# Performance work log

Hardware: AMD Instinct MI355X
Metric: run time of the kernel (lower is better)

## Reference

```python
import jax, jax.numpy as jnp
import numpy as np

N_NODES = 100000
NEG_SLOPE = 0.2  # PyG GATConv default


def gat_conv(x, src, dst, W, a_src, a_dst, n_nodes):
    """One PyG-style GATConv (with self-loops already appended to src/dst).
    x: [N, Fin], W: [Fin, H*C], a_src/a_dst: [H, C]. Returns [N, H, C]."""
    H, C = a_src.shape
    h = (x @ W).reshape(-1, H, C)                      # [N, H, C]
    s_src = jnp.einsum('nhc,hc->nh', h, a_src)         # [N, H]
    s_dst = jnp.einsum('nhc,hc->nh', h, a_dst)         # [N, H]
    e = jax.nn.leaky_relu(s_src[src] + s_dst[dst], NEG_SLOPE)  # [E, H]
    # segment softmax over incoming edges of each destination node
    e_max = jax.ops.segment_max(e, dst, num_segments=n_nodes)  # [N, H]
    e_exp = jnp.exp(e - e_max[dst])
    denom = jax.ops.segment_sum(e_exp, dst, num_segments=n_nodes)
    alpha = e_exp / (denom[dst] + 1e-16)               # [E, H]
    msg = h[src] * alpha[:, :, None]                   # [E, H, C]
    return jax.ops.segment_sum(msg, dst, num_segments=n_nodes)  # [N, H, C]


def setup_inputs() -> dict:
    key = jax.random.key(0)
    ks = jax.random.split(key, 10)
    in_dim, hidden, heads, out_dim = 128, 32, 4, 32
    N, E = N_NODES, 1600000
    x = jax.random.normal(ks[0], (N, in_dim), dtype=jnp.float32)
    edge_index = jax.random.randint(ks[1], (2, E), 0, N, dtype=jnp.int64)
    s = 0.1
    return {
        'x': x,
        'edge_index': edge_index,
        'W1': s * jax.random.normal(ks[2], (in_dim, heads * hidden), dtype=jnp.float32),
        'a_src1': s * jax.random.normal(ks[3], (heads, hidden), dtype=jnp.float32),
        'a_dst1': s * jax.random.normal(ks[4], (heads, hidden), dtype=jnp.float32),
        'b1': jnp.zeros((heads * hidden,), dtype=jnp.float32),
        'W2': s * jax.random.normal(ks[5], (heads * hidden, out_dim), dtype=jnp.float32),
        'a_src2': s * jax.random.normal(ks[6], (1, out_dim), dtype=jnp.float32),
        'a_dst2': s * jax.random.normal(ks[7], (1, out_dim), dtype=jnp.float32),
        'b2': jnp.zeros((out_dim,), dtype=jnp.float32),
    }


def reference(x, edge_index, W1, a_src1, a_dst1, b1, W2, a_src2, a_dst2, b2):
    N = x.shape[0]
    loops = jnp.arange(N, dtype=edge_index.dtype)
    src = jnp.concatenate([edge_index[0], loops])  # PyG adds self-loops
    dst = jnp.concatenate([edge_index[1], loops])
    h1 = gat_conv(x, src, dst, W1, a_src1, a_dst1, N)      # [N, H, C]
    h1 = jax.nn.elu(h1.reshape(N, -1) + b1)                # concat heads + bias, elu
    h2 = gat_conv(h1, src, dst, W2, a_src2, a_dst2, N)     # [N, 1, out]
    return h2.mean(axis=1) + b2                            # concat=False -> mean over heads
```

## Files before the change

kernel.cpp:

```cpp
#include <hip/hip_runtime.h>
#include <hip/hip_bf16.h>

#define NEG 0.2f
#define BK_SHIFT 9
#define BK_CAP 9216

typedef short short8 __attribute__((ext_vector_type(8)));
typedef float f32x4 __attribute__((ext_vector_type(4)));

__device__ __forceinline__ float lrelu(float x){ return x > 0.f ? x : NEG * x; }
__device__ __forceinline__ float elu_f(float x){ return x > 0.f ? x : expm1f(x); }
__device__ __forceinline__ unsigned short f2bf(float f){
  unsigned int u = __float_as_uint(f);
  unsigned int r = u + 0x7fffu + ((u >> 16) & 1u);
  return (unsigned short)(r >> 16);
}
__device__ __forceinline__ float bf2f(unsigned short u){
  return __uint_as_float(((unsigned int)u) << 16);
}

__global__ __launch_bounds__(256) void k_binA(
    const int* __restrict__ src, const int* __restrict__ dst, int E,
    int* __restrict__ gcursor, int2* __restrict__ ebuf){
  __shared__ int hist[256];
  __shared__ int base[256];
  int t = threadIdx.x;
  hist[t] = 0;
  __syncthreads();
  int e0 = blockIdx.x * 4096;
  for (int j = 0; j < 16; j++){
    int e = e0 + j * 256 + t;
    if (e < E) atomicAdd(&hist[dst[e] >> BK_SHIFT], 1);
  }
  __syncthreads();
  int cnt = hist[t];
  if (cnt > 0) base[t] = atomicAdd(&gcursor[t], cnt);
  hist[t] = 0;
  __syncthreads();
  for (int j = 0; j < 16; j++){
    int e = e0 + j * 256 + t;
    if (e < E){
      int d = dst[e]; int b = d >> BK_SHIFT;
      int loc = atomicAdd(&hist[b], 1);
      ebuf[(size_t)b * BK_CAP + base[b] + loc] = make_int2(src[e], d);
    }
  }
}

__global__ __launch_bounds__(256) void k_bscan(
    const int* __restrict__ gcount, int* __restrict__ bbase,
    int* __restrict__ rowp, int N, int NBK, int total){
  __shared__ int sd[256];
  int t = threadIdx.x;
  int nodes = 0;
  if (t < NBK){ int nb = N - (t << BK_SHIFT); nodes = nb > 512 ? 512 : nb; }
  int v = (t < NBK) ? gcount[t] + nodes : 0;
  sd[t] = v; __syncthreads();
  for (int off = 1; off < 256; off <<= 1){
    int x = (t >= off) ? sd[t - off] : 0;
    __syncthreads(); sd[t] += x; __syncthreads();
  }
  if (t < NBK) bbase[t] = sd[t] - v;
  if (t == 0) rowp[N] = total;
}

__global__ __launch_bounds__(256) void k_csrB2(
    const int2* __restrict__ ebuf, const int* __restrict__ gcount,
    const int* __restrict__ bbase, int* __restrict__ rowp,
    int* __restrict__ csr, int N){
  __shared__ int hist[512];
  __shared__ int psum[256];
  int b = blockIdx.x, t = threadIdx.x;
  int nbase = b << BK_SHIFT;
  int cnt = gcount[b];
  const int2* eb = ebuf + (size_t)b * BK_CAP;
  hist[t] = 0; hist[t + 256] = 0;
  __syncthreads();
  for (int i = t; i < cnt; i += 256)
    atomicAdd(&hist[eb[i].y - nbase], 1);
  __syncthreads();
  int v0 = hist[2 * t], v1 = hist[2 * t + 1];
  int ps = v0 + v1;
  psum[t] = ps; __syncthreads();
  for (int off = 1; off < 256; off <<= 1){
    int x = (t >= off) ? psum[t - off] : 0;
    __syncthreads(); psum[t] += x; __syncthreads();
  }
  int eo = psum[t] - ps;
  int bb = bbase[b];
  int n0 = 2 * t, n1 = 2 * t + 1;
  int r0 = bb + eo + n0;
  int r1 = bb + eo + v0 + n1;
  if (nbase + n0 < N) rowp[nbase + n0] = r0;
  if (nbase + n1 < N) rowp[nbase + n1] = r1;
  __syncthreads();
  hist[n0] = r0; hist[n1] = r1;
  __syncthreads();
  for (int i = t; i < cnt; i += 256){
    int2 e = eb[i];
    int pos = atomicAdd(&hist[e.y - nbase], 1);
    csr[pos] = e.x;
  }
  __syncthreads();
  if (nbase + n0 < N) csr[hist[n0]] = nbase + n0;
  if (nbase + n1 < N) csr[hist[n1]] = nbase + n1;
}

__global__ __launch_bounds__(256, 3) void k_gemm1(
    const float* __restrict__ x, const float* __restrict__ W,
    const float* __restrict__ a_src, const float* __restrict__ a_dst,
    unsigned short* __restrict__ h_bf, float* __restrict__ ss, float* __restrict__ sd, int N){
  __shared__ unsigned short Wt[128 * 136];
  __shared__ unsigned short Xb[64 * 136];
  int t = threadIdx.x;
  int rb = blockIdx.x * 64;

  {
    int n = t & 127, kh = (t >> 7) << 6;
    #pragma unroll
    for (int j = 0; j < 16; j++){
      int k0 = kh + j * 4;
      float w0 = W[(size_t)(k0 + 0) * 128 + n];
      float w1 = W[(size_t)(k0 + 1) * 128 + n];
      float w2 = W[(size_t)(k0 + 2) * 128 + n];
      float w3 = W[(size_t)(k0 + 3) * 128 + n];
      uint2 pk;
      pk.x = ((unsigned)f2bf(w1) << 16) | f2bf(w0);
      pk.y = ((unsigned)f2bf(w3) << 16) | f2bf(w2);
      *(uint2*)&Wt[n * 136 + k0] = pk;
    }
  }
  #pragma unroll
  for (int j = 0; j < 8; j++){
    int fi = j * 256 + t;
    int row = fi >> 5, k4 = (fi & 31) * 4;
    int gr = rb + row;
    float4 v = make_float4(0.f, 0.f, 0.f, 0.f);
    if (gr < N) v = *(const float4*)&x[(size_t)gr * 128 + k4];
    uint2 pk;
    pk.x = ((unsigned)f2bf(v.y) << 16) | f2bf(v.x);
    pk.y = ((unsigned)f2bf(v.w) << 16) | f2bf(v.z);
    *(uint2*)&Xb[row * 136 + k4] = pk;
  }
  __syncthreads();

  int w = t >> 6, l = t & 63;
  int m = l & 15, quad = l >> 4;
  f32x4 acc[8];
  #pragma unroll
  for (int ct = 0; ct < 8; ct++) acc[ct] = (f32x4){0.f, 0.f, 0.f, 0.f};

  #pragma unroll
  for (int kc = 0; kc < 4; kc++){
    short8 a = *(const short8*)&Xb[(w * 16 + m) * 136 + kc * 32 + quad * 8];
    #pragma unroll
    for (int ct = 0; ct < 8; ct++){
      short8 b = *(const short8*)&Wt[(ct * 16 + m) * 136 + kc * 32 + quad * 8];
      acc[ct] = __builtin_amdgcn_mfma_f32_16x16x32_bf16(a, b, acc[ct], 0, 0, 0);
    }
  }

  float as[8], ad[8];
  #pragma unroll
  for (int ct = 0; ct < 8; ct++){ as[ct] = a_src[ct * 16 + m]; ad[ct] = a_dst[ct * 16 + m]; }

  #pragma unroll
  for (int reg = 0; reg < 4; reg++){
    int gr = rb + w * 16 + quad * 4 + reg;
    bool ok = gr < N;
    if (ok){
      #pragma unroll
      for (int ct = 0; ct < 8; ct++)
        h_bf[(size_t)gr * 128 + ct * 16 + m] = f2bf(acc[ct][reg]);
    }
    #pragma unroll
    for (int hh = 0; hh < 4; hh++){
      float ps = acc[2*hh][reg] * as[2*hh] + acc[2*hh+1][reg] * as[2*hh+1];
      float pd = acc[2*hh][reg] * ad[2*hh] + acc[2*hh+1][reg] * ad[2*hh+1];
      ps += __shfl_xor(ps, 1, 16); ps += __shfl_xor(ps, 2, 16);
      ps += __shfl_xor(ps, 4, 16); ps += __shfl_xor(ps, 8, 16);
      pd += __shfl_xor(pd, 1, 16); pd += __shfl_xor(pd, 2, 16);
      pd += __shfl_xor(pd, 4, 16); pd += __shfl_xor(pd, 8, 16);
      if (m == 0 && ok){ ss[(size_t)gr * 4 + hh] = ps; sd[(size_t)gr * 4 + hh] = pd; }
    }
  }
}

__global__ __launch_bounds__(256) void k_agg1(
    const int* __restrict__ row_ptr, const int* __restrict__ csr_src,
    const float* __restrict__ ss, const float* __restrict__ sdst,
    const __hip_bfloat162* __restrict__ hb2,
    unsigned int* __restrict__ out1_bf, int N){
  int n = blockIdx.x * 4 + (threadIdx.x >> 6);
  if (n >= N) return;
  int l = threadIdx.x & 63;
  int hd = l >> 4;
  float sdv = sdst[(size_t)n * 4 + hd];
  int j8 = l & 7, hh8 = (l >> 3) & 3;
  float sw8 = sdst[(size_t)n * 4 + hh8];
  int j4 = l & 3, hh4 = (l >> 2) & 3;
  float sw4 = sdst[(size_t)n * 4 + hh4];
  int beg = row_ptr[n], end = row_ptr[n + 1];
  float ax = 0.f, ay = 0.f, sw = 0.f;
  int e = beg;
  for (; e + 8 <= end; e += 8){
    int sj = csr_src[e + j8];
    float wv = __expf(lrelu(ss[(size_t)sj * 4 + hh8] + sw8));
    int s0 = __shfl(sj, 0, 8), s1 = __shfl(sj, 1, 8), s2 = __shfl(sj, 2, 8), s3 = __shfl(sj, 3, 8);
    int s4 = __shfl(sj, 4, 8), s5 = __shfl(sj, 5, 8), s6 = __shfl(sj, 6, 8), s7 = __shfl(sj, 7, 8);
    float w0 = __shfl(wv, hd * 8 + 0, 32), w1 = __shfl(wv, hd * 8 + 1, 32);
    float w2 = __shfl(wv, hd * 8 + 2, 32), w3 = __shfl(wv, hd * 8 + 3, 32);
    float w4 = __shfl(wv, hd * 8 + 4, 32), w5 = __shfl(wv, hd * 8 + 5, 32);
    float w6 = __shfl(wv, hd * 8 + 6, 32), w7 = __shfl(wv, hd * 8 + 7, 32);
    float2 v0 = __bfloat1622float2(hb2[(size_t)s0 * 64 + l]);
    float2 v1 = __bfloat1622float2(hb2[(size_t)s1 * 64 + l]);
    float2 v2 = __bfloat1622float2(hb2[(size_t)s2 * 64 + l]);
    float2 v3 = __bfloat1622float2(hb2[(size_t)s3 * 64 + l]);
    float2 v4 = __bfloat1622float2(hb2[(size_t)s4 * 64 + l]);
    float2 v5 = __bfloat1622float2(hb2[(size_t)s5 * 64 + l]);
    float2 v6 = __bfloat1622float2(hb2[(size_t)s6 * 64 + l]);
    float2 v7 = __bfloat1622float2(hb2[(size_t)s7 * 64 + l]);
    ax += w0*v0.x + w1*v1.x + w2*v2.x + w3*v3.x + w4*v4.x + w5*v5.x + w6*v6.x + w7*v7.x;
    ay += w0*v0.y + w1*v1.y + w2*v2.y + w3*v3.y + w4*v4.y + w5*v5.y + w6*v6.y + w7*v7.y;
    sw += w0 + w1 + w2 + w3 + w4 + w5 + w6 + w7;
  }
  for (; e + 4 <= end; e += 4){
    int sj = csr_src[e + j4];
    float wv = __expf(lrelu(ss[(size_t)sj * 4 + hh4] + sw4));
    int s0 = __shfl(sj, 0, 4), s1 = __shfl(sj, 1, 4);
    int s2 = __shfl(sj, 2, 4), s3 = __shfl(sj, 3, 4);
    float w0 = __shfl(wv, hd * 4 + 0, 16), w1 = __shfl(wv, hd * 4 + 1, 16);
    float w2 = __shfl(wv, hd * 4 + 2, 16), w3 = __shfl(wv, hd * 4 + 3, 16);
    float2 v0 = __bfloat1622float2(hb2[(size_t)s0 * 64 + l]);
    float2 v1 = __bfloat1622float2(hb2[(size_t)s1 * 64 + l]);
    float2 v2 = __bfloat1622float2(hb2[(size_t)s2 * 64 + l]);
    float2 v3 = __bfloat1622float2(hb2[(size_t)s3 * 64 + l]);
    ax += w0*v0.x + w1*v1.x + w2*v2.x + w3*v3.x;
    ay += w0*v0.y + w1*v1.y + w2*v2.y + w3*v3.y;
    sw += w0 + w1 + w2 + w3;
  }
  for (; e < end; e++){
    int s = csr_src[e];
    float w = __expf(lrelu(ss[(size_t)s * 4 + hd] + sdv));
    float2 v = __bfloat1622float2(hb2[(size_t)s * 64 + l]);
    ax += w*v.x; ay += w*v.y; sw += w;
  }
  float inv = 1.f / (sw + 1e-16f);
  unsigned int lo = f2bf(ax * inv), hi = f2bf(ay * inv);
  out1_bf[(size_t)n * 64 + l] = (hi << 16) | lo;
}

__global__ __launch_bounds__(256) void k_gemm2(
    const unsigned int* __restrict__ out1_bf, const float* __restrict__ b1,
    const float* __restrict__ W2,
    const float* __restrict__ a_src, const float* __restrict__ a_dst,
    unsigned short* __restrict__ h2_bf, float* __restrict__ s_src2, float* __restrict__ s_dst2, int N){
  __shared__ __align__(16) float Wl[128 * 32];
  __shared__ __align__(16) float Xl[64 * 132];
  int t = threadIdx.x;
  int rb = blockIdx.x * 64;

  const float4* Wg4 = (const float4*)W2;
  float4* Wl4 = (float4*)Wl;
  #pragma unroll
  for (int j = 0; j < 4; j++) Wl4[j * 256 + t] = Wg4[j * 256 + t];

  #pragma unroll
  for (int j = 0; j < 4; j++){
    int fi = j * 256 + t;
    int row = fi >> 4, q = fi & 15;
    int gr = rb + row;
    float v[8] = {0.f,0.f,0.f,0.f,0.f,0.f,0.f,0.f};
    if (gr < N){
      uint4 u = *(const uint4*)&out1_bf[(size_t)gr * 64 + q * 4];
      float4 bva = *(const float4*)&b1[q * 8];
      float4 bvb = *(const float4*)&b1[q * 8 + 4];
      v[0] = elu_f(bf2f((unsigned short)(u.x & 0xffff)) + bva.x);
      v[1] = elu_f(bf2f((unsigned short)(u.x >> 16))    + bva.y);
      v[2] = elu_f(bf2f((unsigned short)(u.y & 0xffff)) + bva.z);
      v[3] = elu_f(bf2f((unsigned short)(u.y >> 16))    + bva.w);
      v[4] = elu_f(bf2f((unsigned short)(u.z & 0xffff)) + bvb.x);
      v[5] = elu_f(bf2f((unsigned short)(u.z >> 16))    + bvb.y);
      v[6] = elu_f(bf2f((unsigned short)(u.w & 0xffff)) + bvb.z);
      v[7] = elu_f(bf2f((unsigned short)(u.w >> 16))    + bvb.w);
    }
    #pragma unroll
    for (int i = 0; i < 8; i++) Xl[row * 132 + q * 8 + i] = v[i];
  }
  __syncthreads();

  int cg = t & 7, rg = t >> 3;
  int c0 = cg * 4, r0 = rg * 2;
  float acc[2][4] = {};

  #pragma unroll 8
  for (int k = 0; k < 128; k++){
    float a0 = Xl[r0 * 132 + k];
    float a1 = Xl[(r0 + 1) * 132 + k];
    float4 b = *(float4*)&Wl[k * 32 + c0];
    acc[0][0] += a0 * b.x; acc[0][1] += a0 * b.y; acc[0][2] += a0 * b.z; acc[0][3] += a0 * b.w;
    acc[1][0] += a1 * b.x; acc[1][1] += a1 * b.y; acc[1][2] += a1 * b.z; acc[1][3] += a1 * b.w;
  }

  float as[4], ad[4];
  #pragma unroll
  for (int j = 0; j < 4; j++){ as[j] = a_src[c0 + j]; ad[j] = a_dst[c0 + j]; }
  #pragma unroll
  for (int i = 0; i < 2; i++){
    int row = rb + r0 + i;
    if (row < N){
      ushort4 o;
      o.x = f2bf(acc[i][0]); o.y = f2bf(acc[i][1]); o.z = f2bf(acc[i][2]); o.w = f2bf(acc[i][3]);
      *(ushort4*)&h2_bf[(size_t)row * 32 + c0] = o;
    }
    float ps = 0.f, pd = 0.f;
    #pragma unroll
    for (int j = 0; j < 4; j++){ ps += acc[i][j] * as[j]; pd += acc[i][j] * ad[j]; }
    ps += __shfl_xor(ps, 1, 8); ps += __shfl_xor(ps, 2, 8); ps += __shfl_xor(ps, 4, 8);
    pd += __shfl_xor(pd, 1, 8); pd += __shfl_xor(pd, 2, 8); pd += __shfl_xor(pd, 4, 8);
    if ((t & 7) == 0 && row < N){ s_src2[row] = ps; s_dst2[row] = pd; }
  }
}

__global__ __launch_bounds__(256) void k_agg2(
    const int* __restrict__ row_ptr, const int* __restrict__ csr_src,
    const float* __restrict__ ss2, const float* __restrict__ sd2,
    const unsigned short* __restrict__ h2bf, const float* __restrict__ b2,
    float* __restrict__ out, int N){
  int n = blockIdx.x * 8 + (threadIdx.x >> 5);
  if (n >= N) return;
  int c = threadIdx.x & 31;
  float sdv = sd2[n];
  int beg = row_ptr[n], end = row_ptr[n + 1];
  float acc = 0.f, sw = 0.f;
  int e = beg;
  for (; e + 4 <= end; e += 4){
    int s0 = csr_src[e], s1 = csr_src[e+1], s2 = csr_src[e+2], s3 = csr_src[e+3];
    int sj = csr_src[e + (c & 3)];
    float wv = __expf(lrelu(ss2[sj] + sdv));
    float w0 = __shfl(wv, 0, 4), w1 = __shfl(wv, 1, 4);
    float w2 = __shfl(wv, 2, 4), w3 = __shfl(wv, 3, 4);
    float v0 = bf2f(h2bf[(size_t)s0 * 32 + c]);
    float v1 = bf2f(h2bf[(size_t)s1 * 32 + c]);
    float v2 = bf2f(h2bf[(size_t)s2 * 32 + c]);
    float v3 = bf2f(h2bf[(size_t)s3 * 32 + c]);
    acc += w0*v0 + w1*v1 + w2*v2 + w3*v3;
    sw += w0 + w1 + w2 + w3;
  }
  for (; e < end; e++){
    int s = csr_src[e];
    float w = __expf(lrelu(ss2[s] + sdv));
    acc += w * bf2f(h2bf[(size_t)s * 32 + c]);
    sw += w;
  }
  out[(size_t)n * 32 + c] = acc / (sw + 1e-16f) + b2[c];
}

extern "C" void kernel_launch(void* const* d_in, const int* in_sizes, int n_in,
                              void* d_out, int out_size, void* d_ws, size_t ws_size,
                              hipStream_t stream) {
  const float* x      = (const float*)d_in[0];
  const int*   ei     = (const int*)  d_in[1];
  const float* W1     = (const float*)d_in[2];
  const float* a_src1 = (const float*)d_in[3];
  const float* a_dst1 = (const float*)d_in[4];
  const float* b1     = (const float*)d_in[5];
  const float* W2     = (const float*)d_in[6];
  const float* a_src2 = (const float*)d_in[7];
  const float* a_dst2 = (const float*)d_in[8];
  const float* b2     = (const float*)d_in[9];
  float* out = (float*)d_out;

  int N = in_sizes[0] / 128;
  int E = in_sizes[1] / 2;
  const int* srcp = ei;
  const int* dstp = ei + E;
  int total = E + N;
  int NBK = (N + 511) >> 9;

  char* p = (char*)d_ws;
  auto alloc = [&](size_t bytes) -> void* {
    void* r = (void*)p; p += (bytes + 255) & ~(size_t)255; return r;
  };
  unsigned short* h_bf    = (unsigned short*)alloc((size_t)N * 128 * 2);
  unsigned int*   out1_bf = (unsigned int*)alloc((size_t)N * 64 * 4);
  unsigned short* h2_bf   = (unsigned short*)alloc((size_t)N * 32 * 2);
  float* ss1  = (float*)alloc((size_t)N * 4 * 4);
  float* sd1  = (float*)alloc((size_t)N * 4 * 4);
  float* ss2  = (float*)alloc((size_t)N * 4);
  float* sd2  = (float*)alloc((size_t)N * 4);
  int* rowp   = (int*)alloc((size_t)(N + 1) * 4);
  int* csr    = (int*)alloc((size_t)total * 4);
  int* bbase  = (int*)alloc(256 * 4);
  int* gcur   = (int*)alloc(256 * 4);
  int2* ebuf  = (int2*)out1_bf;
  (void)ws_size; (void)n_in; (void)out_size;

  hipMemsetAsync(gcur, 0, 256 * 4, stream);
  k_binA<<<(E + 4095) / 4096, 256, 0, stream>>>(srcp, dstp, E, gcur, ebuf);
  k_bscan<<<1, 256, 0, stream>>>(gcur, bbase, rowp, N, NBK, total);
  k_csrB2<<<NBK, 256, 0, stream>>>(ebuf, gcur, bbase, rowp, csr, N);

  k_gemm1<<<(N + 63) / 64, 256, 0, stream>>>(x, W1, a_src1, a_dst1, h_bf, ss1, sd1, N);
  k_agg1<<<(N + 3) / 4, 256, 0, stream>>>(rowp, csr, ss1, sd1, (const __hip_bfloat162*)h_bf, out1_bf, N);
  k_gemm2<<<(N + 63) / 64, 256, 0, stream>>>(out1_bf, b1, W2, a_src2, a_dst2, h2_bf, ss2, sd2, N);
  k_agg2<<<(N + 7) / 8, 256, 0, stream>>>(rowp, csr, ss2, sd2, h2_bf, b2, out, N);
}
```

Baseline: 331.2 us.

## Fuse bucket scan into CSR build, prepack W1, widen binning and agg2 unroll

Removes the single-block bucket scan kernel by having every CSR-build block redo the small 256-entry scan itself, and raises that kernel to 1024 threads. Binning now uses 512-thread blocks. W1 is converted to transposed bf16 once by a new small kernel so each gemm1 block copies it with vector loads instead of doing strided fp32 loads and conversion. agg2 gains an 8-edge unrolled path that loads each source index once and shares it by shuffle. These changes aim to cut launch count, serial scan latency and redundant per-block work, at the cost of an extra tiny kernel and repeated scans.

```diff
diff --git a/kernel.cpp b/kernel.cpp
--- a/kernel.cpp
+++ b/kernel.cpp
@@ -19,26 +19,28 @@
   return __uint_as_float(((unsigned int)u) << 16);
 }
 
-__global__ __launch_bounds__(256) void k_binA(
+__global__ __launch_bounds__(512) void k_binA(
     const int* __restrict__ src, const int* __restrict__ dst, int E,
     int* __restrict__ gcursor, int2* __restrict__ ebuf){
   __shared__ int hist[256];
   __shared__ int base[256];
   int t = threadIdx.x;
-  hist[t] = 0;
+  if (t < 256) hist[t] = 0;
   __syncthreads();
   int e0 = blockIdx.x * 4096;
-  for (int j = 0; j < 16; j++){
-    int e = e0 + j * 256 + t;
+  for (int j = 0; j < 8; j++){
+    int e = e0 + j * 512 + t;
     if (e < E) atomicAdd(&hist[dst[e] >> BK_SHIFT], 1);
   }
   __syncthreads();
-  int cnt = hist[t];
-  if (cnt > 0) base[t] = atomicAdd(&gcursor[t], cnt);
-  hist[t] = 0;
-  __syncthreads();
-  for (int j = 0; j < 16; j++){
-    int e = e0 + j * 256 + t;
+  if (t < 256){
+    int cnt = hist[t];
+    if (cnt > 0) base[t] = atomicAdd(&gcursor[t], cnt);
+    hist[t] = 0;
+  }
+  __syncthreads();
+  for (int j = 0; j < 8; j++){
+    int e = e0 + j * 512 + t;
     if (e < E){
       int d = dst[e]; int b = d >> BK_SHIFT;
       int loc = atomicAdd(&hist[b], 1);
@@ -47,67 +49,75 @@
   }
 }
 
-__global__ __launch_bounds__(256) void k_bscan(
-    const int* __restrict__ gcount, int* __restrict__ bbase,
-    int* __restrict__ rowp, int N, int NBK, int total){
-  __shared__ int sd[256];
-  int t = threadIdx.x;
-  int nodes = 0;
-  if (t < NBK){ int nb = N - (t << BK_SHIFT); nodes = nb > 512 ? 512 : nb; }
-  int v = (t < NBK) ? gcount[t] + nodes : 0;
-  sd[t] = v; __syncthreads();
-  for (int off = 1; off < 256; off <<= 1){
-    int x = (t >= off) ? sd[t - off] : 0;
-    __syncthreads(); sd[t] += x; __syncthreads();
-  }
-  if (t < NBK) bbase[t] = sd[t] - v;
-  if (t == 0) rowp[N] = total;
-}
-
-__global__ __launch_bounds__(256) void k_csrB2(
+__global__ __launch_bounds__(1024) void k_csrC(
     const int2* __restrict__ ebuf, const int* __restrict__ gcount,
-    const int* __restrict__ bbase, int* __restrict__ rowp,
-    int* __restrict__ csr, int N){
+    int* __restrict__ rowp, int* __restrict__ csr, int N, int NBK, int total){
   __shared__ int hist[512];
   __shared__ int psum[256];
+  __shared__ int bsum[256];
   int b = blockIdx.x, t = threadIdx.x;
   int nbase = b << BK_SHIFT;
   int cnt = gcount[b];
   const int2* eb = ebuf + (size_t)b * BK_CAP;
-  hist[t] = 0; hist[t + 256] = 0;
-  __syncthreads();
-  for (int i = t; i < cnt; i += 256)
+  if (t < 512) hist[t] = 0;
+  int bv = 0;
+  if (t < 256){
+    int nodes = 0;
+    if (t < NBK){ int nb = N - (t << BK_SHIFT); nodes = nb > 512 ? 512 : nb; bv = gcount[t] + nodes; }
+    bsum[t] = bv;
+  }
+  __syncthreads();
+  for (int off = 1; off < 256; off <<= 1){
+    int x = (t >= off && t < 256) ? bsum[t - off] : 0;
+    __syncthreads();
+    if (t < 256) bsum[t] += x;
+    __syncthreads();
+  }
+  for (int i = t; i < cnt; i += 1024)
     atomicAdd(&hist[eb[i].y - nbase], 1);
   __syncthreads();
-  int v0 = hist[2 * t], v1 = hist[2 * t + 1];
-  int ps = v0 + v1;
-  psum[t] = ps; __syncthreads();
+  int v0 = 0, v1 = 0, ps = 0;
+  if (t < 256){ v0 = hist[2 * t]; v1 = hist[2 * t + 1]; ps = v0 + v1; psum[t] = ps; }
+  __syncthreads();
   for (int off = 1; off < 256; off <<= 1){
-    int x = (t >= off) ? psum[t - off] : 0;
-    __syncthreads(); psum[t] += x; __syncthreads();
-  }
-  int eo = psum[t] - ps;
-  int bb = bbase[b];
-  int n0 = 2 * t, n1 = 2 * t + 1;
-  int r0 = bb + eo + n0;
-  int r1 = bb + eo + v0 + n1;
-  if (nbase + n0 < N) rowp[nbase + n0] = r0;
-  if (nbase + n1 < N) rowp[nbase + n1] = r1;
-  __syncthreads();
-  hist[n0] = r0; hist[n1] = r1;
-  __syncthreads();
-  for (int i = t; i < cnt; i += 256){
+    int x = (t >= off && t < 256) ? psum[t - off] : 0;
+    __syncthreads();
+    if (t < 256) psum[t] += x;
+    __syncthreads();
+  }
+  if (t < 256){
+    int eo = psum[t] - ps;
+    int bb = (b == 0) ? 0 : bsum[b - 1];
+    int n0 = 2 * t, n1 = 2 * t + 1;
+    int r0 = bb + eo + n0;
+    int r1 = bb + eo + v0 + n1;
+    if (nbase + n0 < N) rowp[nbase + n0] = r0;
+    if (nbase + n1 < N) rowp[nbase + n1] = r1;
+    hist[n0] = r0; hist[n1] = r1;
+  }
+  if (b == 0 && t == 0) rowp[N] = total;
+  __syncthreads();
+  for (int i = t; i < cnt; i += 1024){
     int2 e = eb[i];
     int pos = atomicAdd(&hist[e.y - nbase], 1);
     csr[pos] = e.x;
   }
   __syncthreads();
-  if (nbase + n0 < N) csr[hist[n0]] = nbase + n0;
-  if (nbase + n1 < N) csr[hist[n1]] = nbase + n1;
+  if (t < 256){
+    int n0 = 2 * t, n1 = 2 * t + 1;
+    if (nbase + n0 < N) csr[hist[n0]] = nbase + n0;
+    if (nbase + n1 < N) csr[hist[n1]] = nbase + n1;
+  }
+}
+
+__global__ __launch_bounds__(128) void k_packW(
+    const float* __restrict__ W, unsigned short* __restrict__ Wp){
+  int n = blockIdx.x, k = threadIdx.x;
+  Wp[n * 128 + k] = f2bf(W[(size_t)k * 128 + n]);
 }
 
 __global__ __launch_bounds__(256, 3) void k_gemm1(
-    const float* __restrict__ x, const float* __restrict__ W,
+    const float* __restrict__ x, const unsigned short* __restrict__ Wp,
     const float* __restrict__ a_src, const float* __restrict__ a_dst,
     unsigned short* __restrict__ h_bf, float* __restrict__ ss, float* __restrict__ sd, int N){
   __shared__ unsigned short Wt[128 * 136];
@@ -115,20 +125,11 @@
   int t = threadIdx.x;
   int rb = blockIdx.x * 64;
 
-  {
-    int n = t & 127, kh = (t >> 7) << 6;
-    #pragma unroll
-    for (int j = 0; j < 16; j++){
-      int k0 = kh + j * 4;
-      float w0 = W[(size_t)(k0 + 0) * 128 + n];
-      float w1 = W[(size_t)(k0 + 1) * 128 + n];
-      float w2 = W[(size_t)(k0 + 2) * 128 + n];
-      float w3 = W[(size_t)(k0 + 3) * 128 + n];
-      uint2 pk;
-      pk.x = ((unsigned)f2bf(w1) << 16) | f2bf(w0);
-      pk.y = ((unsigned)f2bf(w3) << 16) | f2bf(w2);
-      *(uint2*)&Wt[n * 136 + k0] = pk;
-    }
+  #pragma unroll
+  for (int j = 0; j < 8; j++){
+    int fi = j * 256 + t;
+    int n = fi >> 4, ch = fi & 15;
+    *(uint4*)&Wt[n * 136 + ch * 8] = *(const uint4*)&Wp[n * 128 + ch * 8];
   }
   #pragma unroll
   for (int j = 0; j < 8; j++){
@@ -334,6 +335,25 @@
   int beg = row_ptr[n], end = row_ptr[n + 1];
   float acc = 0.f, sw = 0.f;
   int e = beg;
+  int j8 = c & 7;
+  for (; e + 8 <= end; e += 8){
+    int sj = csr_src[e + j8];
+    float wv = __expf(lrelu(ss2[sj] + sdv));
+    int s0 = __shfl(sj, 0, 8), s1 = __shfl(sj, 1, 8), s2 = __shfl(sj, 2, 8), s3 = __shfl(sj, 3, 8);
+    int s4 = __shfl(sj, 4, 8), s5 = __shfl(sj, 5, 8), s6 = __shfl(sj, 6, 8), s7 = __shfl(sj, 7, 8);
+    float w0 = __shfl(wv, 0, 8), w1 = __shfl(wv, 1, 8), w2 = __shfl(wv, 2, 8), w3 = __shfl(wv, 3, 8);
+    float w4 = __shfl(wv, 4, 8), w5 = __shfl(wv, 5, 8), w6 = __shfl(wv, 6, 8), w7 = __shfl(wv, 7, 8);
+    float v0 = bf2f(h2bf[(size_t)s0 * 32 + c]);
+    float v1 = bf2f(h2bf[(size_t)s1 * 32 + c]);
+    float v2 = bf2f(h2bf[(size_t)s2 * 32 + c]);
+    float v3 = bf2f(h2bf[(size_t)s3 * 32 + c]);
+    float v4 = bf2f(h2bf[(size_t)s4 * 32 + c]);
+    float v5 = bf2f(h2bf[(size_t)s5 * 32 + c]);
+    float v6 = bf2f(h2bf[(size_t)s6 * 32 + c]);
+    float v7 = bf2f(h2bf[(size_t)s7 * 32 + c]);
+    acc += w0*v0 + w1*v1 + w2*v2 + w3*v3 + w4*v4 + w5*v5 + w6*v6 + w7*v7;
+    sw += w0 + w1 + w2 + w3 + w4 + w5 + w6 + w7;
+  }
   for (; e + 4 <= end; e += 4){
     int s0 = csr_src[e], s1 = csr_src[e+1], s2 = csr_src[e+2], s3 = csr_src[e+3];
     int sj = csr_src[e + (c & 3)];
@@ -385,23 +405,23 @@
   unsigned short* h_bf    = (unsigned short*)alloc((size_t)N * 128 * 2);
   unsigned int*   out1_bf = (unsigned int*)alloc((size_t)N * 64 * 4);
   unsigned short* h2_bf   = (unsigned short*)alloc((size_t)N * 32 * 2);
+  unsigned short* Wp      = (unsigned short*)alloc(128 * 128 * 2);
   float* ss1  = (float*)alloc((size_t)N * 4 * 4);
   float* sd1  = (float*)alloc((size_t)N * 4 * 4);
   float* ss2  = (float*)alloc((size_t)N * 4);
   float* sd2  = (float*)alloc((size_t)N * 4);
   int* rowp   = (int*)alloc((size_t)(N + 1) * 4);
   int* csr    = (int*)alloc((size_t)total * 4);
-  int* bbase  = (int*)alloc(256 * 4);
   int* gcur   = (int*)alloc(256 * 4);
   int2* ebuf  = (int2*)out1_bf;
   (void)ws_size; (void)n_in; (void)out_size;
 
   hipMemsetAsync(gcur, 0, 256 * 4, stream);
-  k_binA<<<(E + 4095) / 4096, 256, 0, stream>>>(srcp, dstp, E, gcur, ebuf);
-  k_bscan<<<1, 256, 0, stream>>>(gcur, bbase, rowp, N, NBK, total);
-  k_csrB2<<<NBK, 256, 0, stream>>>(ebuf, gcur, bbase, rowp, csr, N);
-
-  k_gemm1<<<(N + 63) / 64, 256, 0, stream>>>(x, W1, a_src1, a_dst1, h_bf, ss1, sd1, N);
+  k_binA<<<(E + 4095) / 4096, 512, 0, stream>>>(srcp, dstp, E, gcur, ebuf);
+  k_csrC<<<NBK, 1024, 0, stream>>>(ebuf, gcur, rowp, csr, N, NBK, total);
+
+  k_packW<<<128, 128, 0, stream>>>(W1, Wp);
+  k_gemm1<<<(N + 63) / 64, 256, 0, stream>>>(x, Wp, a_src1, a_dst1, h_bf, ss1, sd1, N);
   k_agg1<<<(N + 3) / 4, 256, 0, stream>>>(rowp, csr, ss1, sd1, (const __hip_bfloat162*)h_bf, out1_bf, N);
   k_gemm2<<<(N + 63) / 64, 256, 0, stream>>>(out1_bf, b1, W2, a_src2, a_dst2, h2_bf, ss2, sd2, N);
   k_agg2<<<(N + 7) / 8, 256, 0, stream>>>(rowp, csr, ss2, sd2, h2_bf, b2, out, N);
```

Result: faster. 310.4 us (-6.3%).
